# Performance work log

Hardware: AMD Instinct MI355X
Metric: run time of the kernel (lower is better)

## Reference

```python
import jax, jax.numpy as jnp
import numpy as np

NEG_CAUSAL = -1e10  # matches torch buffer triu(ones*-1e10, diag=1)
NEG_PAD = -10000.0
NUM_HEADS = 16


def setup_inputs() -> dict:
    key = jax.random.key(0)
    ks = jax.random.split(key, 6)
    B, S, D = 2, 2048, 1024
    scale = 0.02
    return {
        "hidden_states": jax.random.normal(ks[0], (B, S, D), jnp.float32),
        "attention_mask": jnp.ones((B, S), jnp.float32),
        "Wq": jax.random.normal(ks[1], (D, D), jnp.float32) * scale,
        "bq": jnp.zeros((D,), jnp.float32),
        "Wk": jax.random.normal(ks[2], (D, D), jnp.float32) * scale,
        "bk": jnp.zeros((D,), jnp.float32),
        "Wv": jax.random.normal(ks[3], (D, D), jnp.float32) * scale,
        "bv": jnp.zeros((D,), jnp.float32),
        "Wo": jax.random.normal(ks[4], (D, D), jnp.float32) * scale,
        "bo": jnp.zeros((D,), jnp.float32),
    }


def reference(hidden_states, attention_mask, Wq, bq, Wk, bk, Wv, bv, Wo, bo):
    B, S, D = hidden_states.shape
    H = NUM_HEADS
    hd = D // H

    def heads(x):  # [B,S,D] -> [B,H,S,hd]
        return x.reshape(B, S, H, hd).transpose(0, 2, 1, 3)

    q = heads(hidden_states @ Wq + bq)
    k = heads(hidden_states @ Wk + bk)
    v = heads(hidden_states @ Wv + bv)

    scores = jnp.einsum("bhqd,bhkd->bhqk", q, k) / jnp.sqrt(jnp.float32(hd))
    causal = jnp.triu(jnp.full((S, S), NEG_CAUSAL, jnp.float32), k=1)
    scores = scores + causal
    # additive padding mask: (1 - m) * -10000, broadcast over heads and query pos
    scores = scores + (1.0 - attention_mask)[:, None, None, :] * NEG_PAD

    probs = jax.nn.softmax(scores, axis=-1)
    # dropout p=0.1 is inactive in eval mode (training=False)
    ctx = jnp.einsum("bhqk,bhkd->bhqd", probs, v)
    ctx = ctx.transpose(0, 2, 1, 3).reshape(B, S, D)
    return ctx @ Wo + bo
```

## Files before the change

kernel.cpp:

```cpp
#include <hip/hip_runtime.h>

typedef __attribute__((ext_vector_type(8))) short short8_t;
typedef __attribute__((ext_vector_type(4))) float float4_t;
typedef unsigned short u16;
typedef unsigned int u32;
typedef unsigned long long u64;

__device__ inline u16 f2bf(float x) {
  union { float f; u32 u; } v; v.f = x;
  u32 r = v.u + 0x7FFFu + ((v.u >> 16) & 1u);
  return (u16)(r >> 16);
}
__device__ inline u32 packbf(float a, float b) {
  return (u32)f2bf(a) | ((u32)f2bf(b) << 16);
}
__device__ inline void async16(const u16* g, u16* l) {
  __builtin_amdgcn_global_load_lds(
      (const __attribute__((address_space(1))) unsigned int*)g,
      (__attribute__((address_space(3))) unsigned int*)l, 16, 0, 0);
}

__global__ __launch_bounds__(256) void prologue(const float* __restrict__ X,
                                                const float* __restrict__ Wq, const float* __restrict__ Wk,
                                                const float* __restrict__ Wv, const float* __restrict__ Wo,
                                                u16* __restrict__ Xb, u16* __restrict__ WqkvT,
                                                u16* __restrict__ WoT) {
  __shared__ float tls[32][33];
  int bid = blockIdx.x;
  if (bid < 4096) {
    int i = bid * 256 + threadIdx.x;
    float4_t x = ((const float4_t*)X)[i];
    union { u32 u[2]; u64 ll; } o;
    o.u[0] = packbf(x[0], x[1]);
    o.u[1] = packbf(x[2], x[3]);
    ((u64*)Xb)[i] = o.ll;
  } else {
    int t = bid - 4096;
    int mat = t >> 10, tile = t & 1023;
    const float* W = (mat == 0) ? Wq : (mat == 1) ? Wk : (mat == 2) ? Wv : Wo;
    u16* WT = (mat < 3) ? WqkvT + ((size_t)mat << 20) : WoT;
    int tx = threadIdx.x & 31, ty = threadIdx.x >> 5;
    int c0 = (tile & 31) * 32, r0 = (tile >> 5) * 32;
    #pragma unroll
    for (int i = 0; i < 4; ++i)
      tls[ty + i * 8][tx] = W[(r0 + ty + i * 8) * 1024 + c0 + tx];
    __syncthreads();
    #pragma unroll
    for (int i = 0; i < 4; ++i)
      WT[(size_t)(c0 + ty + i * 8) * 1024 + r0 + tx] = f2bf(tls[tx][ty + i * 8]);
  }
}

__global__ __launch_bounds__(256) void gemm128(const u16* __restrict__ A, const u16* __restrict__ BT,
                                               const float* __restrict__ bias0, const float* __restrict__ bias1,
                                               const float* __restrict__ bias2,
                                               void* __restrict__ o0, void* __restrict__ o1, void* __restrict__ o2,
                                               int mode) {
  __shared__ __align__(16) u16 Als[128 * 64];
  __shared__ __align__(16) u16 Bls[128 * 64];
  int g = blockIdx.x, m0t, n0t;
  if (mode == 4) {
    int mh = g / 384, r = g - mh * 384;
    n0t = r >> 4;
    m0t = mh * 16 + (r & 15);
  } else {
    m0t = g & 31;
    n0t = g >> 5;
  }
  const int m0 = m0t * 128, n0 = n0t * 128;
  const int lane = threadIdx.x & 63, wave = threadIdx.x >> 6;
  const int quad = lane >> 4, c = lane & 15;
  const int wm = wave >> 1, wn = wave & 1;

  const int srow = lane >> 3, schunk = lane & 7;
  int soff[4];  u16 *lA[4], *lB[4];
  #pragma unroll
  for (int q = 0; q < 4; ++q) {
    int r = wave * 32 + q * 8 + srow;
    soff[q] = r * 1024 + ((schunk ^ (r & 7)) << 3);
    lA[q] = &Als[(wave * 32 + q * 8) * 64 + lane * 8];
    lB[q] = &Bls[(wave * 32 + q * 8) * 64 + lane * 8];
  }
  const u16* gA = A + (size_t)m0 * 1024;
  const u16* gB = BT + (size_t)n0 * 1024;

  int ar[2][4], br[2][4];
  #pragma unroll
  for (int ko = 0; ko < 2; ++ko) {
    #pragma unroll
    for (int i = 0; i < 4; ++i) {
      int rowa = wm * 64 + i * 16 + c;
      ar[ko][i] = rowa * 64 + (((ko * 4 + quad) ^ (rowa & 7)) << 3);
      int rowb = wn * 64 + i * 16 + c;
      br[ko][i] = rowb * 64 + (((ko * 4 + quad) ^ (rowb & 7)) << 3);
    }
  }

  float4_t acc[4][4] = {};
  for (int k0 = 0; k0 < 1024; k0 += 64) {
    #pragma unroll
    for (int q = 0; q < 4; ++q) async16(gA + soff[q] + k0, lA[q]);
    #pragma unroll
    for (int q = 0; q < 4; ++q) async16(gB + soff[q] + k0, lB[q]);
    __syncthreads();
    #pragma unroll
    for (int ko = 0; ko < 2; ++ko) {
      short8_t af[4], bfr[4];
      #pragma unroll
      for (int i = 0; i < 4; ++i) af[i] = *(const short8_t*)&Als[ar[ko][i]];
      #pragma unroll
      for (int j = 0; j < 4; ++j) bfr[j] = *(const short8_t*)&Bls[br[ko][j]];
      #pragma unroll
      for (int i = 0; i < 4; ++i)
        #pragma unroll
        for (int j = 0; j < 4; ++j)
          acc[i][j] = __builtin_amdgcn_mfma_f32_16x16x32_bf16(af[i], bfr[j], acc[i][j], 0, 0, 0);
    }
    __syncthreads();
  }

  const int mrow = m0 + wm * 64, ncol = n0 + wn * 64;
  if (mode == 3) {
    float* o = (float*)o0;
    #pragma unroll
    for (int i = 0; i < 4; ++i) {
      #pragma unroll
      for (int j = 0; j < 4; ++j) {
        int colb = ncol + j * 16 + c;
        float bv = bias0[colb];
        int rowb = mrow + i * 16 + quad * 4;
        #pragma unroll
        for (int r = 0; r < 4; ++r)
          o[(size_t)(rowb + r) * 1024 + colb] = acc[i][j][r] + bv;
      }
    }
  } else {
    #pragma unroll
    for (int j = 0; j < 4; ++j) {
      int colb = ncol + j * 16 + c;
      int which = colb >> 10;
      int n1 = colb & 1023, h = n1 >> 6, d = n1 & 63;
      const float* bp = (which == 0) ? bias0 : (which == 1 ? bias1 : bias2);
      float bv = bp[n1];
      #pragma unroll
      for (int i = 0; i < 4; ++i) {
        int rowb = mrow + i * 16 + quad * 4;
        int b = rowb >> 11, s = rowb & 2047;
        if (which == 2) {
          u16* o = (u16*)o2 + (((size_t)(b * 16 + h) * 64 + d) * 2048 + s);
          union { u32 u[2]; u64 ll; } ov;
          ov.u[0] = packbf(acc[i][j][0] + bv, acc[i][j][1] + bv);
          ov.u[1] = packbf(acc[i][j][2] + bv, acc[i][j][3] + bv);
          *(u64*)o = ov.ll;
        } else {
          float sc = (which == 0) ? 0.125f : 1.0f;
          u16* o = (u16*)((which == 0) ? o0 : o1);
          #pragma unroll
          for (int r = 0; r < 4; ++r)
            o[(((size_t)(b * 16 + h) * 2048 + (s + r)) << 6) + d] = f2bf((acc[i][j][r] + bv) * sc);
        }
      }
    }
  }
}

__device__ inline void softmax_p(float4_t s0, float4_t s1, float4_t mpl0, float4_t mpl1,
                                 bool diag, int kbase, int quad, int c, int qg,
                                 float& lacc, float* p) {
  const float LOG2E = 1.4426950408889634f;
  #pragma unroll
  for (int e = 0; e < 8; ++e) {
    float sv = (e < 4) ? s0[e] : s1[e - 4];
    float ml = (e < 4) ? mpl0[e] : mpl1[e - 4];
    float arg = __builtin_fmaf(sv, LOG2E, ml);
    if (diag) {
      int kpos = kbase + ((e >> 2) << 4) + quad * 4 + (e & 3);
      arg = (kpos > qg) ? -50.0f : arg;
    }
    float pe = exp2f(arg);
    p[e] = pe;
    lacc += pe;
  }
}

__device__ inline short8_t p_to_b32(const float* p, int quad, int c) {
  u32 pk0[2] = {packbf(p[0], p[1]), packbf(p[2], p[3])};
  u32 pk1[2] = {packbf(p[4], p[5]), packbf(p[6], p[7])};
  int base = ((quad & 1) * 2) * 16 + c;
  union { u32 u[4]; short8_t v; } pf;
  #pragma unroll
  for (int x = 0; x < 4; ++x) {
    int src = base + ((x >> 1) << 4);
    int v0 = __shfl((int)pk0[x & 1], src);
    int v1 = __shfl((int)pk1[x & 1], src);
    pf.u[x] = (quad < 2) ? (u32)v0 : (u32)v1;
  }
  return pf.v;
}

__global__ __launch_bounds__(512) void attn_kernel(const u16* __restrict__ Q, const u16* __restrict__ K,
                                                   const u16* __restrict__ VT, const float* __restrict__ mask,
                                                   u16* __restrict__ ctx) {
  __shared__ float cmb[8][64][17];
  const float C1 = 10000.0f * 1.4426950408889634f;
  int w = threadIdx.x >> 6, lane = threadIdx.x & 63;
  int quad = lane >> 4, c = lane & 15;
  int g = blockIdx.x;
  int bh = (g & 7) * 4 + ((g >> 3) & 3);
  int u = 63 - (g >> 5);
  int b = bh >> 4, h = bh & 15;
  const u16* Kp = K + ((size_t)bh << 17);
  const u16* Vp = VT + ((size_t)bh << 17);
  const float* mp = mask + (b << 11);

  int q0 = u << 5;
  const u16* Qp = Q + (((size_t)bh * 2048 + q0 + c) << 6) + quad * 8;
  short8_t qA0 = *(const short8_t*)(Qp);
  short8_t qA1 = *(const short8_t*)(Qp + 32);
  short8_t qB0 = *(const short8_t*)(Qp + 1024);
  short8_t qB1 = *(const short8_t*)(Qp + 1024 + 32);
  float4_t OA[4] = {}, OB[4] = {};
  float lA = 0.0f, lB = 0.0f;
  int qgA = q0 + c, qgB = q0 + 16 + c;
  for (int t = w; t <= u; t += 8) {
    int kbase = t << 5;
    const u16* kp = Kp + (((size_t)kbase + c) << 6) + quad * 8;
    short8_t ka0 = *(const short8_t*)(kp);
    short8_t ka1 = *(const short8_t*)(kp + 32);
    short8_t kb0 = *(const short8_t*)(kp + 1024);
    short8_t kb1 = *(const short8_t*)(kp + 1024 + 32);
    const u16* vp = Vp + (size_t)c * 2048 + kbase + quad * 8;
    short8_t vf0 = *(const short8_t*)(vp);
    short8_t vf1 = *(const short8_t*)(vp + 16 * 2048);
    short8_t vf2 = *(const short8_t*)(vp + 32 * 2048);
    short8_t vf3 = *(const short8_t*)(vp + 48 * 2048);
    float4_t mv0 = *(const float4_t*)(mp + kbase + quad * 4);
    float4_t mv1 = *(const float4_t*)(mp + kbase + 16 + quad * 4);
    float4_t mpl0 = (mv0 - 1.0f) * C1;
    float4_t mpl1 = (mv1 - 1.0f) * C1;
    bool diag = (t == u);
    float4_t sA0 = {}, sA1 = {}, sB0 = {}, sB1 = {};
    sA0 = __builtin_amdgcn_mfma_f32_16x16x32_bf16(ka0, qA0, sA0, 0, 0, 0);
    sA0 = __builtin_amdgcn_mfma_f32_16x16x32_bf16(ka1, qA1, sA0, 0, 0, 0);
    sA1 = __builtin_amdgcn_mfma_f32_16x16x32_bf16(kb0, qA0, sA1, 0, 0, 0);
    sA1 = __builtin_amdgcn_mfma_f32_16x16x32_bf16(kb1, qA1, sA1, 0, 0, 0);
    sB0 = __builtin_amdgcn_mfma_f32_16x16x32_bf16(ka0, qB0, sB0, 0, 0, 0);
    sB0 = __builtin_amdgcn_mfma_f32_16x16x32_bf16(ka1, qB1, sB0, 0, 0, 0);
    sB1 = __builtin_amdgcn_mfma_f32_16x16x32_bf16(kb0, qB0, sB1, 0, 0, 0);
    sB1 = __builtin_amdgcn_mfma_f32_16x16x32_bf16(kb1, qB1, sB1, 0, 0, 0);
    float pA[8], pB[8];
    softmax_p(sA0, sA1, mpl0, mpl1, diag, kbase, quad, c, qgA, lA, pA);
    softmax_p(sB0, sB1, mpl0, mpl1, diag, kbase, quad, c, qgB, lB, pB);
    short8_t pfA = p_to_b32(pA, quad, c);
    short8_t pfB = p_to_b32(pB, quad, c);
    OA[0] = __builtin_amdgcn_mfma_f32_16x16x32_bf16(vf0, pfA, OA[0], 0, 0, 0);
    OA[1] = __builtin_amdgcn_mfma_f32_16x16x32_bf16(vf1, pfA, OA[1], 0, 0, 0);
    OA[2] = __builtin_amdgcn_mfma_f32_16x16x32_bf16(vf2, pfA, OA[2], 0, 0, 0);
    OA[3] = __builtin_amdgcn_mfma_f32_16x16x32_bf16(vf3, pfA, OA[3], 0, 0, 0);
    OB[0] = __builtin_amdgcn_mfma_f32_16x16x32_bf16(vf0, pfB, OB[0], 0, 0, 0);
    OB[1] = __builtin_amdgcn_mfma_f32_16x16x32_bf16(vf1, pfB, OB[1], 0, 0, 0);
    OB[2] = __builtin_amdgcn_mfma_f32_16x16x32_bf16(vf2, pfB, OB[2], 0, 0, 0);
    OB[3] = __builtin_amdgcn_mfma_f32_16x16x32_bf16(vf3, pfB, OB[3], 0, 0, 0);
  }
  float* cw = &cmb[w][lane][0];
  #pragma unroll
  for (int d = 0; d < 4; ++d)
    #pragma unroll
    for (int r = 0; r < 4; ++r) cw[d * 4 + r] = OA[d][r];
  cw[16] = lA;
  __syncthreads();
  if (w < 4) {
    float4_t s = {};
    float la = 0.0f;
    #pragma unroll
    for (int w2 = 0; w2 < 8; ++w2) {
      const float* cr = &cmb[w2][lane][0];
      #pragma unroll
      for (int r = 0; r < 4; ++r) s[r] += cr[w * 4 + r];
      la += cr[16];
    }
    la += __shfl_xor(la, 16); la += __shfl_xor(la, 32);
    float rA = 1.0f / la;
    u16* op = ctx + ((size_t)(b * 2048 + q0 + c) * 1024 + h * 64 + w * 16 + quad * 4);
    union { u32 uu[2]; u64 ll; } ov;
    ov.uu[0] = packbf(s[0] * rA, s[1] * rA);
    ov.uu[1] = packbf(s[2] * rA, s[3] * rA);
    *(u64*)op = ov.ll;
  }
  __syncthreads();
  #pragma unroll
  for (int d = 0; d < 4; ++d)
    #pragma unroll
    for (int r = 0; r < 4; ++r) cw[d * 4 + r] = OB[d][r];
  cw[16] = lB;
  __syncthreads();
  if (w >= 4) {
    int dblk = w - 4;
    float4_t s = {};
    float lb = 0.0f;
    #pragma unroll
    for (int w2 = 0; w2 < 8; ++w2) {
      const float* cr = &cmb[w2][lane][0];
      #pragma unroll
      for (int r = 0; r < 4; ++r) s[r] += cr[dblk * 4 + r];
      lb += cr[16];
    }
    lb += __shfl_xor(lb, 16); lb += __shfl_xor(lb, 32);
    float rB = 1.0f / lb;
    u16* op = ctx + ((size_t)(b * 2048 + q0 + 16 + c) * 1024 + h * 64 + dblk * 16 + quad * 4);
    union { u32 uu[2]; u64 ll; } ov;
    ov.uu[0] = packbf(s[0] * rB, s[1] * rB);
    ov.uu[1] = packbf(s[2] * rB, s[3] * rB);
    *(u64*)op = ov.ll;
  }
}

extern "C" void kernel_launch(void* const* d_in, const int* in_sizes, int n_in,
                              void* d_out, int out_size, void* d_ws, size_t ws_size,
                              hipStream_t stream) {
  const float* X    = (const float*)d_in[0];
  const float* mask = (const float*)d_in[1];
  const float* Wq   = (const float*)d_in[2];
  const float* bq   = (const float*)d_in[3];
  const float* Wk   = (const float*)d_in[4];
  const float* bk   = (const float*)d_in[5];
  const float* Wv   = (const float*)d_in[6];
  const float* bv   = (const float*)d_in[7];
  const float* Wo   = (const float*)d_in[8];
  const float* bo   = (const float*)d_in[9];

  char* w = (char*)d_ws;
  u16* Xb     = (u16*)(w);
  u16* WqkvT  = (u16*)(w + (8ull  << 20));
  u16* WoT    = (u16*)(w + (14ull << 20));
  u16* Qb     = (u16*)(w + (16ull << 20));
  u16* Kb     = (u16*)(w + (24ull << 20));
  u16* VTb    = (u16*)(w + (32ull << 20));
  u16* Ctx    = (u16*)(w + (40ull << 20));

  prologue<<<8192, 256, 0, stream>>>(X, Wq, Wk, Wv, Wo, Xb, WqkvT, WoT);
  gemm128<<<768, 256, 0, stream>>>(Xb, WqkvT, bq, bk, bv, Qb, Kb, VTb, 4);
  attn_kernel<<<2048, 512, 0, stream>>>(Qb, Kb, VTb, mask, Ctx);
  gemm128<<<256, 256, 0, stream>>>(Ctx, WoT, bo, bo, bo, d_out, d_out, d_out, 3);
}
```

Before: 230.7 us.

## Prefetch next K/V tile in registers and use hardware bf16 pack conversion

The attention loop now double-buffers K and V fragments in registers, loading the next tile before computing on the current one so global load latency overlaps with MFMA and softmax work. The manual round-to-nearest bf16 packing is replaced with the cvt_pk_bf16_f32 builtin when the compiler provides it, which cuts ALU instructions in conversion-heavy paths. Softmax is also restructured: causal masking runs only on the diagonal tile and uses precomputed key offsets. The extra live registers for the prefetched tile raise register pressure and may lower occupancy.

```diff
diff --git a/kernel.cpp b/kernel.cpp
--- a/kernel.cpp
+++ b/kernel.cpp
@@ -11,9 +11,18 @@
   u32 r = v.u + 0x7FFFu + ((v.u >> 16) & 1u);
   return (u16)(r >> 16);
 }
-__device__ inline u32 packbf(float a, float b) {
+#if __has_builtin(__builtin_amdgcn_cvt_pk_bf16_f32)
+typedef __attribute__((ext_vector_type(2))) __bf16 bf162_t;
+__device__ inline u32 pk2(float a, float b) {
+  union { bf162_t v; u32 u; } cv;
+  cv.v = __builtin_amdgcn_cvt_pk_bf16_f32(a, b);
+  return cv.u;
+}
+#else
+__device__ inline u32 pk2(float a, float b) {
   return (u32)f2bf(a) | ((u32)f2bf(b) << 16);
 }
+#endif
 __device__ inline void async16(const u16* g, u16* l) {
   __builtin_amdgcn_global_load_lds(
       (const __attribute__((address_space(1))) unsigned int*)g,
@@ -31,8 +40,8 @@
     int i = bid * 256 + threadIdx.x;
     float4_t x = ((const float4_t*)X)[i];
     union { u32 u[2]; u64 ll; } o;
-    o.u[0] = packbf(x[0], x[1]);
-    o.u[1] = packbf(x[2], x[3]);
+    o.u[0] = pk2(x[0], x[1]);
+    o.u[1] = pk2(x[2], x[3]);
     ((u64*)Xb)[i] = o.ll;
   } else {
     int t = bid - 4096;
@@ -149,8 +158,8 @@
         if (which == 2) {
           u16* o = (u16*)o2 + (((size_t)(b * 16 + h) * 64 + d) * 2048 + s);
           union { u32 u[2]; u64 ll; } ov;
-          ov.u[0] = packbf(acc[i][j][0] + bv, acc[i][j][1] + bv);
-          ov.u[1] = packbf(acc[i][j][2] + bv, acc[i][j][3] + bv);
+          ov.u[0] = pk2(acc[i][j][0] + bv, acc[i][j][1] + bv);
+          ov.u[1] = pk2(acc[i][j][2] + bv, acc[i][j][3] + bv);
           *(u64*)o = ov.ll;
         } else {
           float sc = (which == 0) ? 0.125f : 1.0f;
@@ -164,28 +173,9 @@
   }
 }
 
-__device__ inline void softmax_p(float4_t s0, float4_t s1, float4_t mpl0, float4_t mpl1,
-                                 bool diag, int kbase, int quad, int c, int qg,
-                                 float& lacc, float* p) {
-  const float LOG2E = 1.4426950408889634f;
-  #pragma unroll
-  for (int e = 0; e < 8; ++e) {
-    float sv = (e < 4) ? s0[e] : s1[e - 4];
-    float ml = (e < 4) ? mpl0[e] : mpl1[e - 4];
-    float arg = __builtin_fmaf(sv, LOG2E, ml);
-    if (diag) {
-      int kpos = kbase + ((e >> 2) << 4) + quad * 4 + (e & 3);
-      arg = (kpos > qg) ? -50.0f : arg;
-    }
-    float pe = exp2f(arg);
-    p[e] = pe;
-    lacc += pe;
-  }
-}
-
 __device__ inline short8_t p_to_b32(const float* p, int quad, int c) {
-  u32 pk0[2] = {packbf(p[0], p[1]), packbf(p[2], p[3])};
-  u32 pk1[2] = {packbf(p[4], p[5]), packbf(p[6], p[7])};
+  u32 pk0[2] = {pk2(p[0], p[1]), pk2(p[2], p[3])};
+  u32 pk1[2] = {pk2(p[4], p[5]), pk2(p[6], p[7])};
   int base = ((quad & 1) * 2) * 16 + c;
   union { u32 u[4]; short8_t v; } pf;
   #pragma unroll
@@ -198,11 +188,31 @@
   return pf.v;
 }
 
+struct KV {
+  short8_t ka0, ka1, kb0, kb1, v0, v1, v2, v3;
+};
+__device__ inline KV load_kv(const u16* __restrict__ Kp, const u16* __restrict__ Vp,
+                             int kbase, int quad, int c) {
+  KV r;
+  const u16* kp = Kp + (((size_t)kbase + c) << 6) + quad * 8;
+  r.ka0 = *(const short8_t*)(kp);
+  r.ka1 = *(const short8_t*)(kp + 32);
+  r.kb0 = *(const short8_t*)(kp + 1024);
+  r.kb1 = *(const short8_t*)(kp + 1024 + 32);
+  const u16* vp = Vp + (size_t)c * 2048 + kbase + quad * 8;
+  r.v0 = *(const short8_t*)(vp);
+  r.v1 = *(const short8_t*)(vp + 16 * 2048);
+  r.v2 = *(const short8_t*)(vp + 32 * 2048);
+  r.v3 = *(const short8_t*)(vp + 48 * 2048);
+  return r;
+}
+
 __global__ __launch_bounds__(512) void attn_kernel(const u16* __restrict__ Q, const u16* __restrict__ K,
                                                    const u16* __restrict__ VT, const float* __restrict__ mask,
                                                    u16* __restrict__ ctx) {
   __shared__ float cmb[8][64][17];
   const float C1 = 10000.0f * 1.4426950408889634f;
+  const float LOG2E = 1.4426950408889634f;
   int w = threadIdx.x >> 6, lane = threadIdx.x & 63;
   int quad = lane >> 4, c = lane & 15;
   int g = blockIdx.x;
@@ -222,45 +232,63 @@
   float4_t OA[4] = {}, OB[4] = {};
   float lA = 0.0f, lB = 0.0f;
   int qgA = q0 + c, qgB = q0 + 16 + c;
+  int ke[8];
+  #pragma unroll
+  for (int e = 0; e < 8; ++e) ke[e] = ((e >> 2) << 4) + quad * 4 + (e & 3);
+
+  KV cur = load_kv(Kp, Vp, w << 5, quad, c);
   for (int t = w; t <= u; t += 8) {
+    int tn = (t + 8 <= u) ? (t + 8) : t;
+    KV nxt = load_kv(Kp, Vp, tn << 5, quad, c);
     int kbase = t << 5;
-    const u16* kp = Kp + (((size_t)kbase + c) << 6) + quad * 8;
-    short8_t ka0 = *(const short8_t*)(kp);
-    short8_t ka1 = *(const short8_t*)(kp + 32);
-    short8_t kb0 = *(const short8_t*)(kp + 1024);
-    short8_t kb1 = *(const short8_t*)(kp + 1024 + 32);
-    const u16* vp = Vp + (size_t)c * 2048 + kbase + quad * 8;
-    short8_t vf0 = *(const short8_t*)(vp);
-    short8_t vf1 = *(const short8_t*)(vp + 16 * 2048);
-    short8_t vf2 = *(const short8_t*)(vp + 32 * 2048);
-    short8_t vf3 = *(const short8_t*)(vp + 48 * 2048);
     float4_t mv0 = *(const float4_t*)(mp + kbase + quad * 4);
     float4_t mv1 = *(const float4_t*)(mp + kbase + 16 + quad * 4);
     float4_t mpl0 = (mv0 - 1.0f) * C1;
     float4_t mpl1 = (mv1 - 1.0f) * C1;
-    bool diag = (t == u);
     float4_t sA0 = {}, sA1 = {}, sB0 = {}, sB1 = {};
-    sA0 = __builtin_amdgcn_mfma_f32_16x16x32_bf16(ka0, qA0, sA0, 0, 0, 0);
-    sA0 = __builtin_amdgcn_mfma_f32_16x16x32_bf16(ka1, qA1, sA0, 0, 0, 0);
-    sA1 = __builtin_amdgcn_mfma_f32_16x16x32_bf16(kb0, qA0, sA1, 0, 0, 0);
-    sA1 = __builtin_amdgcn_mfma_f32_16x16x32_bf16(kb1, qA1, sA1, 0, 0, 0);
-    sB0 = __builtin_amdgcn_mfma_f32_16x16x32_bf16(ka0, qB0, sB0, 0, 0, 0);
-    sB0 = __builtin_amdgcn_mfma_f32_16x16x32_bf16(ka1, qB1, sB0, 0, 0, 0);
-    sB1 = __builtin_amdgcn_mfma_f32_16x16x32_bf16(kb0, qB0, sB1, 0, 0, 0);
-    sB1 = __builtin_amdgcn_mfma_f32_16x16x32_bf16(kb1, qB1, sB1, 0, 0, 0);
+    sA0 = __builtin_amdgcn_mfma_f32_16x16x32_bf16(cur.ka0, qA0, sA0, 0, 0, 0);
+    sA0 = __builtin_amdgcn_mfma_f32_16x16x32_bf16(cur.ka1, qA1, sA0, 0, 0, 0);
+    sA1 = __builtin_amdgcn_mfma_f32_16x16x32_bf16(cur.kb0, qA0, sA1, 0, 0, 0);
+    sA1 = __builtin_amdgcn_mfma_f32_16x16x32_bf16(cur.kb1, qA1, sA1, 0, 0, 0);
+    sB0 = __builtin_amdgcn_mfma_f32_16x16x32_bf16(cur.ka0, qB0, sB0, 0, 0, 0);
+    sB0 = __builtin_amdgcn_mfma_f32_16x16x32_bf16(cur.ka1, qB1, sB0, 0, 0, 0);
+    sB1 = __builtin_amdgcn_mfma_f32_16x16x32_bf16(cur.kb0, qB0, sB1, 0, 0, 0);
+    sB1 = __builtin_amdgcn_mfma_f32_16x16x32_bf16(cur.kb1, qB1, sB1, 0, 0, 0);
     float pA[8], pB[8];
-    softmax_p(sA0, sA1, mpl0, mpl1, diag, kbase, quad, c, qgA, lA, pA);
-    softmax_p(sB0, sB1, mpl0, mpl1, diag, kbase, quad, c, qgB, lB, pB);
+    #pragma unroll
+    for (int e = 0; e < 8; ++e) {
+      float svA = (e < 4) ? sA0[e] : sA1[e - 4];
+      float svB = (e < 4) ? sB0[e] : sB1[e - 4];
+      float ml = (e < 4) ? mpl0[e] : mpl1[e - 4];
+      pA[e] = __builtin_fmaf(svA, LOG2E, ml);
+      pB[e] = __builtin_fmaf(svB, LOG2E, ml);
+    }
+    if (t == u) {
+      int thrA = qgA - kbase, thrB = qgB - kbase;
+      #pragma unroll
+      for (int e = 0; e < 8; ++e) {
+        pA[e] = (ke[e] > thrA) ? -50.0f : pA[e];
+        pB[e] = (ke[e] > thrB) ? -50.0f : pB[e];
+      }
+    }
+    #pragma unroll
+    for (int e = 0; e < 8; ++e) {
+      float peA = exp2f(pA[e]);
+      float peB = exp2f(pB[e]);
+      pA[e] = peA; lA += peA;
+      pB[e] = peB; lB += peB;
+    }
     short8_t pfA = p_to_b32(pA, quad, c);
     short8_t pfB = p_to_b32(pB, quad, c);
-    OA[0] = __builtin_amdgcn_mfma_f32_16x16x32_bf16(vf0, pfA, OA[0], 0, 0, 0);
-    OA[1] = __builtin_amdgcn_mfma_f32_16x16x32_bf16(vf1, pfA, OA[1], 0, 0, 0);
-    OA[2] = __builtin_amdgcn_mfma_f32_16x16x32_bf16(vf2, pfA, OA[2], 0, 0, 0);
-    OA[3] = __builtin_amdgcn_mfma_f32_16x16x32_bf16(vf3, pfA, OA[3], 0, 0, 0);
-    OB[0] = __builtin_amdgcn_mfma_f32_16x16x32_bf16(vf0, pfB, OB[0], 0, 0, 0);
-    OB[1] = __builtin_amdgcn_mfma_f32_16x16x32_bf16(vf1, pfB, OB[1], 0, 0, 0);
-    OB[2] = __builtin_amdgcn_mfma_f32_16x16x32_bf16(vf2, pfB, OB[2], 0, 0, 0);
-    OB[3] = __builtin_amdgcn_mfma_f32_16x16x32_bf16(vf3, pfB, OB[3], 0, 0, 0);
+    OA[0] = __builtin_amdgcn_mfma_f32_16x16x32_bf16(cur.v0, pfA, OA[0], 0, 0, 0);
+    OA[1] = __builtin_amdgcn_mfma_f32_16x16x32_bf16(cur.v1, pfA, OA[1], 0, 0, 0);
+    OA[2] = __builtin_amdgcn_mfma_f32_16x16x32_bf16(cur.v2, pfA, OA[2], 0, 0, 0);
+    OA[3] = __builtin_amdgcn_mfma_f32_16x16x32_bf16(cur.v3, pfA, OA[3], 0, 0, 0);
+    OB[0] = __builtin_amdgcn_mfma_f32_16x16x32_bf16(cur.v0, pfB, OB[0], 0, 0, 0);
+    OB[1] = __builtin_amdgcn_mfma_f32_16x16x32_bf16(cur.v1, pfB, OB[1], 0, 0, 0);
+    OB[2] = __builtin_amdgcn_mfma_f32_16x16x32_bf16(cur.v2, pfB, OB[2], 0, 0, 0);
+    OB[3] = __builtin_amdgcn_mfma_f32_16x16x32_bf16(cur.v3, pfB, OB[3], 0, 0, 0);
+    cur = nxt;
   }
   float* cw = &cmb[w][lane][0];
   #pragma unroll
@@ -283,8 +311,8 @@
     float rA = 1.0f / la;
     u16* op = ctx + ((size_t)(b * 2048 + q0 + c) * 1024 + h * 64 + w * 16 + quad * 4);
     union { u32 uu[2]; u64 ll; } ov;
-    ov.uu[0] = packbf(s[0] * rA, s[1] * rA);
-    ov.uu[1] = packbf(s[2] * rA, s[3] * rA);
+    ov.uu[0] = pk2(s[0] * rA, s[1] * rA);
+    ov.uu[1] = pk2(s[2] * rA, s[3] * rA);
     *(u64*)op = ov.ll;
   }
   __syncthreads();
@@ -309,8 +337,8 @@
     float rB = 1.0f / lb;
     u16* op = ctx + ((size_t)(b * 2048 + q0 + 16 + c) * 1024 + h * 64 + dblk * 16 + quad * 4);
     union { u32 uu[2]; u64 ll; } ov;
-    ov.uu[0] = packbf(s[0] * rB, s[1] * rB);
-    ov.uu[1] = packbf(s[2] * rB, s[3] * rB);
+    ov.uu[0] = pk2(s[0] * rB, s[1] * rB);
+    ov.uu[1] = pk2(s[2] * rB, s[3] * rB);
     *(u64*)op = ov.ll;
   }
 }
```

Result: slower. 254.1 us (+10.1%).
